# Optimization experiments

Hardware: AMD Instinct MI355X
Metric: run time of the kernel (lower is better)

## Reference

```python
import jax, jax.numpy as jnp
import numpy as np

N = 50000      # nodes
E = 800000     # edges (avg degree 16)
DIN = 128      # input_dim
DG = 128       # gnn_dim
DCLS = 128     # cls_dim
DOUT = 10      # output_dim
LMDA = 1.0     # rw_lmda
P_DROP = 0.5


def setup_inputs() -> dict:
    key = jax.random.key(0)
    ks = jax.random.split(key, 12)
    x = jax.random.normal(ks[0], (N, DIN), jnp.float32)
    edge_index = jax.random.randint(ks[1], (2, E), 0, N, dtype=jnp.int64)
    edge_weight = jax.random.uniform(ks[2], (E,), jnp.float32)
    def glorot(k, shape):
        lim = np.sqrt(6.0 / (shape[0] + shape[1])).astype(np.float32)
        return jax.random.uniform(k, shape, jnp.float32, -lim, lim)
    return dict(
        x=x, edge_index=edge_index, edge_weight=edge_weight,
        W_lin_in=glorot(ks[3], (DIN, DG)), b_lin_in=jnp.zeros((DG,), jnp.float32),
        W_agg_in=glorot(ks[4], (DG + DIN, DG)), b_agg_in=jnp.zeros((DG,), jnp.float32),
        W_lin_h=glorot(ks[5], (DG, DG)), b_lin_h=jnp.zeros((DG,), jnp.float32),
        W_agg_h=glorot(ks[6], (2 * DG, DG)), b_agg_h=jnp.zeros((DG,), jnp.float32),
        W_mlp1=glorot(ks[7], (DG, DCLS)), b_mlp1=jnp.zeros((DCLS,), jnp.float32),
        W_mlp2=glorot(ks[8], (DCLS, DOUT)), b_mlp2=jnp.zeros((DOUT,), jnp.float32),
    )


def _gs_layer(x, row, col, ew, inv_cnt, W_lin, b_lin, W_agg, b_agg):
    # GS_reweight: message = (1-lmda)*lin(x_j) + lmda*ew*lin(x_j), mean-aggregated
    # at row (flow='target_to_source': gather from col, scatter to row).
    h = x @ W_lin + b_lin                      # [N, DG] (lin before gather == lin(x_j))
    hj = h[col]                                # [E, DG] gather
    m = (1.0 - LMDA) * hj + LMDA * (ew[:, None] * hj)
    agg = jax.ops.segment_sum(m, row, num_segments=N) * inv_cnt[:, None]  # mean
    out = jnp.concatenate([agg, x], axis=-1) @ W_agg + b_agg              # update()
    return jax.nn.relu(out)


def _dropout(x, k):
    mask = jax.random.bernoulli(k, 1.0 - P_DROP, x.shape)
    return jnp.where(mask, x / (1.0 - P_DROP), 0.0)


def reference(x, edge_index, edge_weight,
              W_lin_in, b_lin_in, W_agg_in, b_agg_in,
              W_lin_h, b_lin_h, W_agg_h, b_agg_h,
              W_mlp1, b_mlp1, W_mlp2, b_mlp2):
    row, col = edge_index[0], edge_index[1]
    cnt = jax.ops.segment_sum(jnp.ones((E,), x.dtype), row, num_segments=N)
    inv_cnt = 1.0 / jnp.maximum(cnt, 1.0)     # scatter_mean: empty rows -> 0
    dk = jax.random.split(jax.random.key(42), 3)
    h = _gs_layer(x, row, col, edge_weight, inv_cnt, W_lin_in, b_lin_in, W_agg_in, b_agg_in)
    h = _dropout(jax.nn.relu(h), dk[0])       # relu is idempotent after update's relu
    for i in range(2):                        # layers 2,3 share prop_hidden weights
        h = _gs_layer(h, row, col, edge_weight, inv_cnt, W_lin_h, b_lin_h, W_agg_h, b_agg_h)
        h = _dropout(jax.nn.relu(h), dk[i + 1])
    y = jax.nn.relu(h @ W_mlp1 + b_mlp1) @ W_mlp2 + b_mlp2  # cls_layers=2, bn=False
    return (h, y)
```

## Files before the change

### kernel.cpp

```cpp
#include <hip/hip_runtime.h>
#include <cstdint>
#include <cstddef>


#define N_NODES 50000
#define N_EDGES 800000
#define DGN 128
#define DOUT 10
#define NELEM (N_NODES * DGN)
#define NMASKW (NELEM / 64)
#define NBINS 391
#define TILE 4096
#define NTILES ((N_EDGES + TILE - 1) / TILE)
#define GBF ((N_NODES + 63) / 64)
#define MK_BLOCKS 25000

#define XB_BLK 6250
#define HI_BLK NTILES
#define WC_BLK 128
#define TR_BLK 192
#define R0 XB_BLK
#define R1 (R0 + HI_BLK)
#define R2 (R1 + WC_BLK)
#define R3 (R2 + TR_BLK)
#define MEGA_BLOCKS (R3 + 1)

#define AB_BLOCKS ((N_NODES + 3) / 4)

typedef __attribute__((ext_vector_type(8))) short bf16x8;
typedef __attribute__((ext_vector_type(4))) float f32x4;

__host__ __device__ static inline unsigned short f2bf(float f) {
  union { float f; unsigned u; } c; c.f = f;
  unsigned u = c.u;
  return (unsigned short)((u + 0x7fffu + ((u >> 16) & 1u)) >> 16);
}
__device__ static inline float bflo(unsigned u) { return __uint_as_float(u << 16); }
__device__ static inline float bfhi(unsigned u) { return __uint_as_float(u & 0xffff0000u); }
__device__ static inline float bf2f(unsigned short h) {
  return __uint_as_float(((unsigned)h) << 16);
}

__host__ __device__ static inline void tf2x32(unsigned k0, unsigned k1,
                                              unsigned c0, unsigned c1,
                                              unsigned& o0, unsigned& o1) {
  unsigned ks2 = k0 ^ k1 ^ 0x1BD11BDAu;
  unsigned x0 = c0 + k0;
  unsigned x1 = c1 + k1;
#define TFR(r) { x0 += x1; x1 = (x1 << (r)) | (x1 >> (32 - (r))); x1 ^= x0; }
  TFR(13) TFR(15) TFR(26) TFR(6)
  x0 += k1;  x1 += ks2 + 1u;
  TFR(17) TFR(29) TFR(16) TFR(24)
  x0 += ks2; x1 += k0 + 2u;
  TFR(13) TFR(15) TFR(26) TFR(6)
  x0 += k0;  x1 += k1 + 3u;
  TFR(17) TFR(29) TFR(16) TFR(24)
  x0 += k1;  x1 += ks2 + 4u;
  TFR(13) TFR(15) TFR(26) TFR(6)
  x0 += ks2; x1 += k0 + 5u;
#undef TFR
  o0 = x0; o1 = x1;
}

__device__ static inline void mask_chunk(unsigned long long* __restrict__ gm,
                                         int i, unsigned k0, unsigned k1) {
  unsigned o0, o1;
  tf2x32(k0, k1, 0u, (unsigned)i, o0, o1);
  unsigned long long b = __ballot(((o0 ^ o1) >> 31) == 0u);
  if ((threadIdx.x & 63) == 0) gm[i >> 6] = b;
}

__global__ __launch_bounds__(256) void mega_kernel(
    const float* __restrict__ x, unsigned short* __restrict__ xb,
    const int* __restrict__ ei, int* __restrict__ chist,
    const float* __restrict__ Wli, const float* __restrict__ Wai,
    const float* __restrict__ Wlh, const float* __restrict__ Wah,
    const float* __restrict__ Wm1,
    const float* __restrict__ bli, const float* __restrict__ blh,
    unsigned short* __restrict__ Tai, unsigned short* __restrict__ Tah,
    unsigned short* __restrict__ Tm1,
    float* __restrict__ bvi, float* __restrict__ bvh) {
  __shared__ int h[NBINS];
  const int b = blockIdx.x;
  const int tid = threadIdx.x;

  if (b < R0) {
    int g = b * 256 + tid;
    float4 v = ((const float4*)x)[g];
    ushort4 o;
    o.x = f2bf(v.x); o.y = f2bf(v.y); o.z = f2bf(v.z); o.w = f2bf(v.w);
    ((ushort4*)xb)[g] = o;
  } else if (b < R1) {
    for (int i = tid; i < NBINS; i += 256) h[i] = 0;
    __syncthreads();
    const int e0 = (b - R0) * TILE;
#pragma unroll 4
    for (int j = 0; j < TILE; j += 256) {
      int e = e0 + j + tid;
      if (e < N_EDGES) {
        int r = ei[e];
        r = (r < 0) ? 0 : (r >= N_NODES ? N_NODES - 1 : r);
        atomicAdd(&h[r >> 7], 1);
      }
    }
    __syncthreads();
    for (int i = tid; i < NBINS; i += 256)
      if (h[i]) atomicAdd(&chist[i], h[i]);
  } else if (b < R2) {
    int idx = (b - R1) * 256 + tid;
    int n = idx & 127;
    int k = (idx >> 7) & 127;
    int m = idx >> 14;
    const float* Wl = m ? Wlh : Wli;
    const float* Wa = m ? Wah : Wai;
    unsigned short* T = m ? Tah : Tai;
    float acc = 0.0f;
#pragma unroll 8
    for (int j = 0; j < 128; ++j)
      acc += Wl[k * 128 + j] * Wa[j * 128 + n];
    T[n * 256 + k] = f2bf(acc);
  } else if (b < R3) {
    int j = (b - R2) * 256 + tid;
    if (j < 16384) {
      int kk = j & 127, n = j >> 7;
      Tai[n * 256 + 128 + kk] = f2bf(Wai[(size_t)(128 + kk) * 128 + n]);
    } else if (j < 32768) {
      int q = j - 16384;
      int kk = q & 127, n = q >> 7;
      Tah[n * 256 + 128 + kk] = f2bf(Wah[(size_t)(128 + kk) * 128 + n]);
    } else {
      int q = j - 32768;
      int k = q & 127, n = q >> 7;
      Tm1[n * 128 + k] = f2bf(Wm1[(size_t)k * 128 + n]);
    }
  } else {
    int n = tid & 127;
    const float* bl = (tid < 128) ? bli : blh;
    const float* Wa = (tid < 128) ? Wai : Wah;
    float acc = 0.0f;
    for (int j = 0; j < 128; ++j) acc += bl[j] * Wa[j * 128 + n];
    if (tid < 128) bvi[n] = acc; else bvh[n] = acc;
  }
}

__global__ __launch_bounds__(512) void prefix_kernel(const int* __restrict__ chist,
                                                     int* __restrict__ cbase,
                                                     int* __restrict__ ccursor,
                                                     int* __restrict__ rowptr) {
  __shared__ int s[512];
  const int t = threadIdx.x;
  int v = (t < NBINS) ? chist[t] : 0;
  s[t] = v;
  __syncthreads();
  for (int off = 1; off < 512; off <<= 1) {
    int tv = (t >= off) ? s[t - off] : 0;
    __syncthreads();
    s[t] += tv;
    __syncthreads();
  }
  if (t <= NBINS) {
    int ex = (t == 0) ? 0 : s[t - 1];
    cbase[t] = ex;
    if (t < NBINS) ccursor[t] = ex;
  }
  if (t == 0) rowptr[N_NODES] = N_EDGES;
}

__global__ __launch_bounds__(256) void scatter_kernel(const int* __restrict__ ei,
                                                      const float* __restrict__ ew,
                                                      int* __restrict__ ccursor,
                                                      uint2* __restrict__ pk,
                                                      unsigned long long* __restrict__ mg0,
                                                      unsigned k00, unsigned k01) {
  if (blockIdx.x >= NTILES) {
    mask_chunk(mg0, (blockIdx.x - NTILES) * 256 + threadIdx.x, k00, k01);
    return;
  }
  __shared__ uint2 st[TILE];
  __shared__ unsigned short sbin[TILE];
  __shared__ int h[NBINS];
  __shared__ int base[NBINS];
  __shared__ int gbase[NBINS];
  __shared__ int cur[NBINS];
  __shared__ int sc[512];
  const int tid = threadIdx.x;
  const int e0 = blockIdx.x * TILE;
  const int nt = (N_EDGES - e0 < TILE) ? (N_EDGES - e0) : TILE;

  for (int i = tid; i < NBINS; i += 256) { h[i] = 0; cur[i] = 0; }
  __syncthreads();
  for (int j = tid; j < nt; j += 256) {
    int r = ei[e0 + j];
    r = (r < 0) ? 0 : (r >= N_NODES ? N_NODES - 1 : r);
    atomicAdd(&h[r >> 7], 1);
  }
  __syncthreads();
  sc[tid] = (tid < NBINS) ? h[tid] : 0;
  sc[tid + 256] = (tid + 256 < NBINS) ? h[tid + 256] : 0;
  __syncthreads();
  for (int off = 1; off < 512; off <<= 1) {
    int a0 = (tid >= off) ? sc[tid - off] : 0;
    int a1 = (tid + 256 >= off) ? sc[tid + 256 - off] : 0;
    __syncthreads();
    sc[tid] += a0; sc[tid + 256] += a1;
    __syncthreads();
  }
  if (tid < NBINS) {
    base[tid] = sc[tid] - h[tid];
    if (h[tid]) gbase[tid] = atomicAdd(&ccursor[tid], h[tid]);
  }
  if (tid + 256 < NBINS) {
    base[tid + 256] = sc[tid + 256] - h[tid + 256];
    if (h[tid + 256]) gbase[tid + 256] = atomicAdd(&ccursor[tid + 256], h[tid + 256]);
  }
  __syncthreads();
  for (int j = tid; j < nt; j += 256) {
    int r = ei[e0 + j];
    r = (r < 0) ? 0 : (r >= N_NODES ? N_NODES - 1 : r);
    int c = ei[N_EDGES + e0 + j];
    c = (c < 0) ? 0 : (c >= N_NODES ? N_NODES - 1 : c);
    int bb = r >> 7;
    int slot = base[bb] + atomicAdd(&cur[bb], 1);
    uint2 p;
    p.x = ((unsigned)r << 16) | (unsigned)c;
    p.y = __float_as_uint(ew[e0 + j]);
    st[slot] = p;
    sbin[slot] = (unsigned short)bb;
  }
  __syncthreads();
  for (int j = tid; j < nt; j += 256) {
    int bb = sbin[j];
    pk[gbase[bb] + (j - base[bb])] = st[j];
  }
}

__global__ __launch_bounds__(256) void place_kernel(const int* __restrict__ cbase,
                                                    const uint2* __restrict__ pk,
                                                    uint2* __restrict__ csr,
                                                    int* __restrict__ rowptr,
                                                    float* __restrict__ invc) {
  __shared__ int lcnt[128];
  __shared__ int lpre[128];
  __shared__ int lcur[128];
  __shared__ int sc[128];
  const int b = blockIdx.x;
  const int tid = threadIdx.x;
  const int cb = cbase[b];
  const int n = cbase[b + 1] - cb;
  const int r0 = b << 7;
  const int nr = (N_NODES - r0 < 128) ? (N_NODES - r0) : 128;

  if (tid < 128) { lcnt[tid] = 0; lcur[tid] = 0; }
  __syncthreads();
  for (int i = tid; i < n; i += 256) {
    int r7 = (int)(pk[cb + i].x >> 16) - r0;
    atomicAdd(&lcnt[r7], 1);
  }
  __syncthreads();
  if (tid < 128) sc[tid] = lcnt[tid];
  __syncthreads();
  for (int off = 1; off < 128; off <<= 1) {
    int tv = (tid >= off && tid < 128) ? sc[tid - off] : 0;
    __syncthreads();
    if (tid < 128) sc[tid] += tv;
    __syncthreads();
  }
  if (tid < 128) lpre[tid] = sc[tid] - lcnt[tid];
  __syncthreads();
  if (tid < nr) {
    rowptr[r0 + tid] = cb + lpre[tid];
    int c = lcnt[tid];
    invc[r0 + tid] = 1.0f / (float)(c > 1 ? c : 1);
  }
  for (int i = tid; i < n; i += 256) {
    uint2 p = pk[cb + i];
    int r7 = (int)(p.x >> 16) - r0;
    int slot = cb + lpre[r7] + atomicAdd(&lcur[r7], 1);
    uint2 o;
    o.x = p.x & 0xFFFFu;
    o.y = p.y;
    csr[slot] = o;
  }
}

__global__ __launch_bounds__(256) void agg_kernel(const unsigned short* __restrict__ hlin,
                                                  const int* __restrict__ rowptr,
                                                  const uint2* __restrict__ csr,
                                                  const float* __restrict__ invc,
                                                  unsigned short* __restrict__ agg,
                                                  float* __restrict__ swout) {
  const int r = blockIdx.x * 4 + (threadIdx.x >> 6);
  const int lane = threadIdx.x & 63;
  const int es = lane >> 4;
  const int cg = lane & 15;
  const int start = rowptr[r];
  const int num = rowptr[r + 1] - start;
  const uint4* __restrict__ H = (const uint4*)hlin;

  float a[8] = {0.f, 0.f, 0.f, 0.f, 0.f, 0.f, 0.f, 0.f};
  float ws = 0.f;
  for (int e = 0; e < num; e += 16) {
#pragma unroll
    for (int j = 0; j < 4; ++j) {
      int idx = e + j * 4 + es;
      bool ok = idx < num;
      int idxc = ok ? idx : (num - 1);
      uint2 q = csr[start + idxc];
      float w = ok ? __uint_as_float(q.y) : 0.0f;
      uint4 p = H[(size_t)q.x * 16 + cg];
      ws += w;
      a[0] += w * bflo(p.x); a[1] += w * bfhi(p.x);
      a[2] += w * bflo(p.y); a[3] += w * bfhi(p.y);
      a[4] += w * bflo(p.z); a[5] += w * bfhi(p.z);
      a[6] += w * bflo(p.w); a[7] += w * bfhi(p.w);
    }
  }
#pragma unroll
  for (int k = 0; k < 8; ++k) {
    a[k] += __shfl_xor(a[k], 32);
    a[k] += __shfl_xor(a[k], 16);
  }
  ws += __shfl_xor(ws, 32);
  ws += __shfl_xor(ws, 16);
  const float s = invc[r];
  if (es == 0) {
    uint4 o;
    o.x = (unsigned)f2bf(a[0] * s) | ((unsigned)f2bf(a[1] * s) << 16);
    o.y = (unsigned)f2bf(a[2] * s) | ((unsigned)f2bf(a[3] * s) << 16);
    o.z = (unsigned)f2bf(a[4] * s) | ((unsigned)f2bf(a[5] * s) << 16);
    o.w = (unsigned)f2bf(a[6] * s) | ((unsigned)f2bf(a[7] * s) << 16);
    ((uint4*)agg)[(size_t)r * 16 + cg] = o;
  }
  if (swout && lane == 0) swout[r] = ws * s;
}

template <bool WF32, bool MASKGEN>
__global__ __launch_bounds__(256) void layer_gemm(
    const unsigned short* __restrict__ Agg, const unsigned short* __restrict__ Hin,
    const unsigned short* __restrict__ Wt,
    const float* __restrict__ bvec, const float* __restrict__ bagg,
    const float* __restrict__ sw,
    const unsigned long long* __restrict__ maskw,
    float* __restrict__ outf, unsigned short* __restrict__ outb,
    unsigned long long* __restrict__ gm, unsigned gk0, unsigned gk1) {
  if (MASKGEN && blockIdx.x >= GBF) {
    mask_chunk(gm, (blockIdx.x - GBF) * 256 + threadIdx.x, gk0, gk1);
    return;
  }
  constexpr int LS = 72;
  __shared__ unsigned short Als[64 * LS];
  __shared__ unsigned short Bls[128 * LS];
  const int tid = threadIdx.x;
  const int m0 = blockIdx.x * 64;
  const int lane = tid & 63;
  const int wid = tid >> 6;
  const int wm = (wid >> 1) * 32;
  const int wn = (wid & 1) * 64;
  const int ln = lane & 15;
  const int lh = lane >> 4;
  const int sArow = tid >> 2;
  const int sAk = (tid & 3) * 16;
  const int sBcol = tid >> 1;
  const int sBk = (tid & 1) * 32;
  int arow = m0 + sArow;
  if (arow >= N_NODES) arow = N_NODES - 1;

  f32x4 acc[2][4];
#pragma unroll
  for (int i = 0; i < 2; ++i)
#pragma unroll
    for (int j = 0; j < 4; ++j)
#pragma unroll
      for (int r = 0; r < 4; ++r) acc[i][j][r] = 0.0f;

  for (int kb = 0; kb < 256; kb += 64) {
    const unsigned short* Asrc = (kb < 128) ? Agg : Hin;
    const unsigned short* ap = Asrc + (size_t)arow * 128 + (kb & 127) + sAk;
    unsigned short* al = &Als[sArow * LS + sAk];
    *(uint4*)(al + 0) = *(const uint4*)(ap + 0);
    *(uint4*)(al + 8) = *(const uint4*)(ap + 8);
    const unsigned short* bp = Wt + (size_t)sBcol * 256 + kb + sBk;
    unsigned short* bl = &Bls[sBcol * LS + sBk];
    *(uint4*)(bl + 0)  = *(const uint4*)(bp + 0);
    *(uint4*)(bl + 8)  = *(const uint4*)(bp + 8);
    *(uint4*)(bl + 16) = *(const uint4*)(bp + 16);
    *(uint4*)(bl + 24) = *(const uint4*)(bp + 24);
    __syncthreads();
#pragma unroll
    for (int ks = 0; ks < 64; ks += 32) {
      bf16x8 af[2], bfr[4];
#pragma unroll
      for (int i = 0; i < 2; ++i)
        af[i] = *(const bf16x8*)&Als[(wm + i * 16 + ln) * LS + ks + lh * 8];
#pragma unroll
      for (int j = 0; j < 4; ++j)
        bfr[j] = *(const bf16x8*)&Bls[(wn + j * 16 + ln) * LS + ks + lh * 8];
#pragma unroll
      for (int i = 0; i < 2; ++i)
#pragma unroll
        for (int j = 0; j < 4; ++j)
          acc[i][j] = __builtin_amdgcn_mfma_f32_16x16x32_bf16(af[i], bfr[j], acc[i][j], 0, 0, 0);
    }
    __syncthreads();
  }

  const int lm = lane >> 4;
  float bc[4], b2[4];
#pragma unroll
  for (int j = 0; j < 4; ++j) {
    int col = wn + j * 16 + ln;
    bc[j] = bvec[col];
    b2[j] = bagg[col];
  }
#pragma unroll
  for (int i = 0; i < 2; ++i) {
    const int lr0 = wm + i * 16 + lm * 4;
#pragma unroll
    for (int r = 0; r < 4; ++r) {
      const int row = m0 + lr0 + r;
      if (row >= N_NODES) continue;
      const float swr = sw[row];
      const unsigned long long mw = maskw[(size_t)row * 2 + (wn >> 6)];
#pragma unroll
      for (int j = 0; j < 4; ++j) {
        const int col = wn + j * 16 + ln;
        float v = acc[i][j][r] + swr * bc[j] + b2[j];
        v = fmaxf(v, 0.0f);
        v = ((mw >> (col & 63)) & 1ull) ? 2.0f * v : 0.0f;
        if (WF32) outf[(size_t)row * DGN + col] = v;
        outb[(size_t)row * DGN + col] = f2bf(v);
      }
    }
  }
}

__global__ __launch_bounds__(256) void mlp_gemm(
    const unsigned short* __restrict__ A0,
    const unsigned short* __restrict__ Wt,
    const float* __restrict__ b1,
    const float* __restrict__ W2, const float* __restrict__ b2,
    float* __restrict__ y) {
  constexpr int LS = 72;
  constexpr int LT = 132;
  __shared__ unsigned short Als[64 * LS];
  __shared__ unsigned short Bls[128 * LS];
  __shared__ unsigned short tT[64 * LT];
  __shared__ float Ws[128 * DOUT];
  __shared__ float bs[DOUT];
  const int tid = threadIdx.x;
  const int m0 = blockIdx.x * 64;
  const int lane = tid & 63;
  const int wid = tid >> 6;
  const int wm = (wid >> 1) * 32;
  const int wn = (wid & 1) * 64;
  const int ln = lane & 15;
  const int lh = lane >> 4;
  const int sArow = tid >> 2;
  const int sAk = (tid & 3) * 16;
  const int sBcol = tid >> 1;
  const int sBk = (tid & 1) * 32;
  int arow = m0 + sArow;
  if (arow >= N_NODES) arow = N_NODES - 1;

  for (int i = tid; i < 128 * DOUT; i += 256) Ws[i] = W2[i];
  if (tid < DOUT) bs[tid] = b2[tid];

  f32x4 acc[2][4];
#pragma unroll
  for (int i = 0; i < 2; ++i)
#pragma unroll
    for (int j = 0; j < 4; ++j)
#pragma unroll
      for (int r = 0; r < 4; ++r) acc[i][j][r] = 0.0f;

  for (int kb = 0; kb < 128; kb += 64) {
    const unsigned short* ap = A0 + (size_t)arow * 128 + kb + sAk;
    unsigned short* al = &Als[sArow * LS + sAk];
    *(uint4*)(al + 0) = *(const uint4*)(ap + 0);
    *(uint4*)(al + 8) = *(const uint4*)(ap + 8);
    const unsigned short* bp = Wt + (size_t)sBcol * 128 + kb + sBk;
    unsigned short* bl = &Bls[sBcol * LS + sBk];
    *(uint4*)(bl + 0)  = *(const uint4*)(bp + 0);
    *(uint4*)(bl + 8)  = *(const uint4*)(bp + 8);
    *(uint4*)(bl + 16) = *(const uint4*)(bp + 16);
    *(uint4*)(bl + 24) = *(const uint4*)(bp + 24);
    __syncthreads();
#pragma unroll
    for (int ks = 0; ks < 64; ks += 32) {
      bf16x8 af[2], bfr[4];
#pragma unroll
      for (int i = 0; i < 2; ++i)
        af[i] = *(const bf16x8*)&Als[(wm + i * 16 + ln) * LS + ks + lh * 8];
#pragma unroll
      for (int j = 0; j < 4; ++j)
        bfr[j] = *(const bf16x8*)&Bls[(wn + j * 16 + ln) * LS + ks + lh * 8];
#pragma unroll
      for (int i = 0; i < 2; ++i)
#pragma unroll
        for (int j = 0; j < 4; ++j)
          acc[i][j] = __builtin_amdgcn_mfma_f32_16x16x32_bf16(af[i], bfr[j], acc[i][j], 0, 0, 0);
    }
    __syncthreads();
  }

  const int lm = lane >> 4;
  float bcol[4];
#pragma unroll
  for (int j = 0; j < 4; ++j) bcol[j] = b1[wn + j * 16 + ln];
#pragma unroll
  for (int i = 0; i < 2; ++i) {
    const int lr0 = wm + i * 16 + lm * 4;
#pragma unroll
    for (int r = 0; r < 4; ++r) {
      const int lr = lr0 + r;
#pragma unroll
      for (int j = 0; j < 4; ++j) {
        const int col = wn + j * 16 + ln;
        float v = fmaxf(acc[i][j][r] + bcol[j], 0.0f);
        tT[lr * LT + col] = f2bf(v);
      }
    }
  }
  __syncthreads();

  if (tid < 64) {
    int row = m0 + tid;
    if (row < N_NODES) {
      float a2[DOUT];
#pragma unroll
      for (int c = 0; c < DOUT; ++c) a2[c] = bs[c];
      const unsigned short* tr = &tT[tid * LT];
#pragma unroll 8
      for (int k = 0; k < 128; ++k) {
        float tv = bf2f(tr[k]);
        const float* wr = &Ws[k * DOUT];
#pragma unroll
        for (int c = 0; c < DOUT; ++c) a2[c] += tv * wr[c];
      }
      float* yp = y + (size_t)row * DOUT;
#pragma unroll
      for (int c = 0; c < DOUT; ++c) yp[c] = a2[c];
    }
  }
}

extern "C" void kernel_launch(void* const* d_in, const int* in_sizes, int n_in,
                              void* d_out, int out_size, void* d_ws, size_t ws_size,
                              hipStream_t stream) {
  const float* x        = (const float*)d_in[0];
  const int*   ei       = (const int*)d_in[1];
  const float* ew       = (const float*)d_in[2];
  const float* W_lin_in = (const float*)d_in[3];
  const float* b_lin_in = (const float*)d_in[4];
  const float* W_agg_in = (const float*)d_in[5];
  const float* b_agg_in = (const float*)d_in[6];
  const float* W_lin_h  = (const float*)d_in[7];
  const float* b_lin_h  = (const float*)d_in[8];
  const float* W_agg_h  = (const float*)d_in[9];
  const float* b_agg_h  = (const float*)d_in[10];
  const float* W_mlp1   = (const float*)d_in[11];
  const float* b_mlp1   = (const float*)d_in[12];
  const float* W_mlp2   = (const float*)d_in[13];
  const float* b_mlp2   = (const float*)d_in[14];

  float* hout = (float*)d_out;
  float* yout = hout + (size_t)NELEM;

  char* p = (char*)d_ws;
  auto alloc = [&](size_t bytes) {
    char* q = p;
    p += (bytes + 255) & ~(size_t)255;
    return q;
  };
  int*   chist   = (int*)alloc((size_t)(NBINS + 1) * 4);
  int*   cbase   = (int*)alloc((size_t)(NBINS + 1) * 4);
  int*   ccursor = (int*)alloc((size_t)NBINS * 4);
  int*   rowptr  = (int*)alloc((size_t)(N_NODES + 1) * 4);
  float* invc    = (float*)alloc((size_t)N_NODES * 4);
  float* swv     = (float*)alloc((size_t)N_NODES * 4);
  uint2* pk      = (uint2*)alloc((size_t)N_EDGES * 8);
  uint2* csr     = (uint2*)alloc((size_t)N_EDGES * 8);
  unsigned short* xb   = (unsigned short*)alloc((size_t)NELEM * 2);
  unsigned short* aggb = (unsigned short*)alloc((size_t)NELEM * 2);
  unsigned short* hA   = (unsigned short*)alloc((size_t)NELEM * 2);
  unsigned short* hB   = (unsigned short*)alloc((size_t)NELEM * 2);
  unsigned long long* mw0 = (unsigned long long*)alloc((size_t)NMASKW * 8);
  unsigned long long* mw1 = (unsigned long long*)alloc((size_t)NMASKW * 8);
  unsigned long long* mw2 = (unsigned long long*)alloc((size_t)NMASKW * 8);
  unsigned short* Tai = (unsigned short*)alloc(32768 * 2);
  unsigned short* Tah = (unsigned short*)alloc(32768 * 2);
  unsigned short* Tm1 = (unsigned short*)alloc(16384 * 2);
  float* bvi = (float*)alloc(128 * 4);
  float* bvh = (float*)alloc(128 * 4);

  unsigned dk[3][2];
  for (unsigned i = 0; i < 3; ++i) tf2x32(0u, 42u, 0u, i, dk[i][0], dk[i][1]);

  hipMemsetAsync(chist, 0, (size_t)(NBINS + 1) * 4, stream);
  mega_kernel<<<MEGA_BLOCKS, 256, 0, stream>>>(
      x, xb, ei, chist, W_lin_in, W_agg_in, W_lin_h, W_agg_h, W_mlp1,
      b_lin_in, b_lin_h, Tai, Tah, Tm1, bvi, bvh);

  prefix_kernel<<<1, 512, 0, stream>>>(chist, cbase, ccursor, rowptr);
  scatter_kernel<<<NTILES + MK_BLOCKS, 256, 0, stream>>>(
      ei, ew, ccursor, pk, mw0, dk[0][0], dk[0][1]);
  place_kernel<<<NBINS, 256, 0, stream>>>(cbase, pk, csr, rowptr, invc);

  agg_kernel<<<AB_BLOCKS, 256, 0, stream>>>(xb, rowptr, csr, invc, aggb, swv);
  layer_gemm<false, true><<<GBF + MK_BLOCKS, 256, 0, stream>>>(
      aggb, xb, Tai, bvi, b_agg_in, swv, mw0, nullptr, hA,
      mw1, dk[1][0], dk[1][1]);

  agg_kernel<<<AB_BLOCKS, 256, 0, stream>>>(hA, rowptr, csr, invc, aggb, nullptr);
  layer_gemm<false, true><<<GBF + MK_BLOCKS, 256, 0, stream>>>(
      aggb, hA, Tah, bvh, b_agg_h, swv, mw1, nullptr, hB,
      mw2, dk[2][0], dk[2][1]);

  agg_kernel<<<AB_BLOCKS, 256, 0, stream>>>(hB, rowptr, csr, invc, aggb, nullptr);
  layer_gemm<true, false><<<GBF, 256, 0, stream>>>(
      aggb, hB, Tah, bvh, b_agg_h, swv, mw2, hout, hA,
      nullptr, 0, 0);

  mlp_gemm<<<GBF, 256, 0, stream>>>(hA, Tm1, b_mlp1, W_mlp2, b_mlp2, yout);
}
```

Before: 326.9 us.

## Partition node features into 32-column panels so aggregation gathers stay cache-resident

Stores bf16 node features as four column panels of 32 elements per node (panel-major) instead of row-major 128-wide rows. The aggregation kernel now runs one grid slice per panel, so each slice gathers from a 3.2 MB working set that fits better in L2/LLC. Consumers (layer GEMM A-operand load, outputs, MLP GEMM) are rewritten to read and write the panel layout. The cost is four passes over the CSR edge list and narrower 64-byte gathers per edge.

```diff
diff --git a/kernel.cpp b/kernel.cpp
--- a/kernel.cpp
+++ b/kernel.cpp
@@ -14,6 +14,7 @@
 #define NTILES ((N_EDGES + TILE - 1) / TILE)
 #define GBF ((N_NODES + 63) / 64)
 #define MK_BLOCKS 25000
+#define PSTRIDE (N_NODES * 32)
 
 #define XB_BLK 6250
 #define HI_BLK NTILES
@@ -25,7 +26,9 @@
 #define R3 (R2 + TR_BLK)
 #define MEGA_BLOCKS (R3 + 1)
 
-#define AB_BLOCKS ((N_NODES + 3) / 4)
+#define AGG_RPB 16
+#define AGG_PB (N_NODES / AGG_RPB)
+#define AGG_BLOCKS (4 * AGG_PB)
 
 typedef __attribute__((ext_vector_type(8))) short bf16x8;
 typedef __attribute__((ext_vector_type(4))) float f32x4;
@@ -89,7 +92,9 @@
     float4 v = ((const float4*)x)[g];
     ushort4 o;
     o.x = f2bf(v.x); o.y = f2bf(v.y); o.z = f2bf(v.z); o.w = f2bf(v.w);
-    ((ushort4*)xb)[g] = o;
+    int node = g >> 5;
+    int d0 = (g & 31) << 2;
+    ((ushort4*)xb)[((size_t)(d0 >> 5) * PSTRIDE + (size_t)node * 32 + (d0 & 31)) >> 2] = o;
   } else if (b < R1) {
     for (int i = tid; i < NBINS; i += 256) h[i] = 0;
     __syncthreads();
@@ -283,55 +288,74 @@
   }
 }
 
-__global__ __launch_bounds__(256) void agg_kernel(const unsigned short* __restrict__ hlin,
-                                                  const int* __restrict__ rowptr,
-                                                  const uint2* __restrict__ csr,
-                                                  const float* __restrict__ invc,
-                                                  unsigned short* __restrict__ agg,
-                                                  float* __restrict__ swout) {
-  const int r = blockIdx.x * 4 + (threadIdx.x >> 6);
+__global__ __launch_bounds__(256) void agg_kernel(
+    const unsigned short* __restrict__ hlin,
+    const int* __restrict__ rowptr,
+    const uint2* __restrict__ csr,
+    const float* __restrict__ invc,
+    unsigned short* __restrict__ agg,
+    float* __restrict__ swout) {
+  const int p = blockIdx.x / AGG_PB;
+  const int rb = (blockIdx.x - p * AGG_PB) * AGG_RPB;
   const int lane = threadIdx.x & 63;
-  const int es = lane >> 4;
-  const int cg = lane & 15;
-  const int start = rowptr[r];
-  const int num = rowptr[r + 1] - start;
-  const uint4* __restrict__ H = (const uint4*)hlin;
-
-  float a[8] = {0.f, 0.f, 0.f, 0.f, 0.f, 0.f, 0.f, 0.f};
-  float ws = 0.f;
-  for (int e = 0; e < num; e += 16) {
-#pragma unroll
-    for (int j = 0; j < 4; ++j) {
-      int idx = e + j * 4 + es;
-      bool ok = idx < num;
-      int idxc = ok ? idx : (num - 1);
-      uint2 q = csr[start + idxc];
-      float w = ok ? __uint_as_float(q.y) : 0.0f;
-      uint4 p = H[(size_t)q.x * 16 + cg];
-      ws += w;
-      a[0] += w * bflo(p.x); a[1] += w * bfhi(p.x);
-      a[2] += w * bflo(p.y); a[3] += w * bfhi(p.y);
-      a[4] += w * bflo(p.z); a[5] += w * bfhi(p.z);
-      a[6] += w * bflo(p.w); a[7] += w * bfhi(p.w);
-    }
-  }
-#pragma unroll
-  for (int k = 0; k < 8; ++k) {
-    a[k] += __shfl_xor(a[k], 32);
-    a[k] += __shfl_xor(a[k], 16);
-  }
-  ws += __shfl_xor(ws, 32);
-  ws += __shfl_xor(ws, 16);
-  const float s = invc[r];
-  if (es == 0) {
-    uint4 o;
-    o.x = (unsigned)f2bf(a[0] * s) | ((unsigned)f2bf(a[1] * s) << 16);
-    o.y = (unsigned)f2bf(a[2] * s) | ((unsigned)f2bf(a[3] * s) << 16);
-    o.z = (unsigned)f2bf(a[4] * s) | ((unsigned)f2bf(a[5] * s) << 16);
-    o.w = (unsigned)f2bf(a[6] * s) | ((unsigned)f2bf(a[7] * s) << 16);
-    ((uint4*)agg)[(size_t)r * 16 + cg] = o;
-  }
-  if (swout && lane == 0) swout[r] = ws * s;
+  const int wid = threadIdx.x >> 6;
+  const int half = lane >> 5;
+  const int ec = (lane >> 2) & 7;
+  const int cg = lane & 3;
+  const uint4* __restrict__ H = (const uint4*)hlin + (size_t)p * (N_NODES * 4);
+
+  for (int rr = 0; rr < 2; ++rr) {
+    const int r = rb + wid * 4 + rr * 2 + half;
+    const int start = rowptr[r];
+    const int num = rowptr[r + 1] - start;
+    float a[8] = {0.f, 0.f, 0.f, 0.f, 0.f, 0.f, 0.f, 0.f};
+    float ws = 0.f;
+    for (int e = 0; e < num; e += 16) {
+      const int i1 = e + ec;
+      const int i2 = e + 8 + ec;
+      if (i1 < num) {
+        uint2 q = csr[start + i1];
+        float w = __uint_as_float(q.y);
+        uint4 pv = H[(size_t)q.x * 4 + cg];
+        ws += w;
+        a[0] += w * bflo(pv.x); a[1] += w * bfhi(pv.x);
+        a[2] += w * bflo(pv.y); a[3] += w * bfhi(pv.y);
+        a[4] += w * bflo(pv.z); a[5] += w * bfhi(pv.z);
+        a[6] += w * bflo(pv.w); a[7] += w * bfhi(pv.w);
+      }
+      if (i2 < num) {
+        uint2 q = csr[start + i2];
+        float w = __uint_as_float(q.y);
+        uint4 pv = H[(size_t)q.x * 4 + cg];
+        ws += w;
+        a[0] += w * bflo(pv.x); a[1] += w * bfhi(pv.x);
+        a[2] += w * bflo(pv.y); a[3] += w * bfhi(pv.y);
+        a[4] += w * bflo(pv.z); a[5] += w * bfhi(pv.z);
+        a[6] += w * bflo(pv.w); a[7] += w * bfhi(pv.w);
+      }
+    }
+#pragma unroll
+    for (int k = 0; k < 8; ++k) {
+      a[k] += __shfl_xor(a[k], 4);
+      a[k] += __shfl_xor(a[k], 8);
+      a[k] += __shfl_xor(a[k], 16);
+    }
+    const float s = invc[r];
+    if ((lane & 31) < 4) {
+      uint4 o;
+      o.x = (unsigned)f2bf(a[0] * s) | ((unsigned)f2bf(a[1] * s) << 16);
+      o.y = (unsigned)f2bf(a[2] * s) | ((unsigned)f2bf(a[3] * s) << 16);
+      o.z = (unsigned)f2bf(a[4] * s) | ((unsigned)f2bf(a[5] * s) << 16);
+      o.w = (unsigned)f2bf(a[6] * s) | ((unsigned)f2bf(a[7] * s) << 16);
+      ((uint4*)agg)[(size_t)r * 16 + p * 4 + cg] = o;
+    }
+    if (swout != nullptr && p == 0) {
+      ws += __shfl_xor(ws, 4);
+      ws += __shfl_xor(ws, 8);
+      ws += __shfl_xor(ws, 16);
+      if ((lane & 31) == 0) swout[r] = ws * s;
+    }
+  }
 }
 
 template <bool WF32, bool MASKGEN>
@@ -374,8 +398,13 @@
       for (int r = 0; r < 4; ++r) acc[i][j][r] = 0.0f;
 
   for (int kb = 0; kb < 256; kb += 64) {
-    const unsigned short* Asrc = (kb < 128) ? Agg : Hin;
-    const unsigned short* ap = Asrc + (size_t)arow * 128 + (kb & 127) + sAk;
+    const unsigned short* ap;
+    if (kb < 128) {
+      ap = Agg + (size_t)arow * 128 + kb + sAk;
+    } else {
+      int kk = kb - 128 + sAk;
+      ap = Hin + (size_t)(kk >> 5) * PSTRIDE + (size_t)arow * 32 + (kk & 31);
+    }
     unsigned short* al = &Als[sArow * LS + sAk];
     *(uint4*)(al + 0) = *(const uint4*)(ap + 0);
     *(uint4*)(al + 8) = *(const uint4*)(ap + 8);
@@ -428,7 +457,7 @@
         v = fmaxf(v, 0.0f);
         v = ((mw >> (col & 63)) & 1ull) ? 2.0f * v : 0.0f;
         if (WF32) outf[(size_t)row * DGN + col] = v;
-        outb[(size_t)row * DGN + col] = f2bf(v);
+        outb[(size_t)(col >> 5) * PSTRIDE + (size_t)row * 32 + (col & 31)] = f2bf(v);
       }
     }
   }
@@ -474,7 +503,9 @@
       for (int r = 0; r < 4; ++r) acc[i][j][r] = 0.0f;
 
   for (int kb = 0; kb < 128; kb += 64) {
-    const unsigned short* ap = A0 + (size_t)arow * 128 + kb + sAk;
+    int kk = kb + sAk;
+    const unsigned short* ap =
+        A0 + (size_t)(kk >> 5) * PSTRIDE + (size_t)arow * 32 + (kk & 31);
     unsigned short* al = &Als[sArow * LS + sAk];
     *(uint4*)(al + 0) = *(const uint4*)(ap + 0);
     *(uint4*)(al + 8) = *(const uint4*)(ap + 8);
@@ -606,17 +637,17 @@
       ei, ew, ccursor, pk, mw0, dk[0][0], dk[0][1]);
   place_kernel<<<NBINS, 256, 0, stream>>>(cbase, pk, csr, rowptr, invc);
 
-  agg_kernel<<<AB_BLOCKS, 256, 0, stream>>>(xb, rowptr, csr, invc, aggb, swv);
+  agg_kernel<<<AGG_BLOCKS, 256, 0, stream>>>(xb, rowptr, csr, invc, aggb, swv);
   layer_gemm<false, true><<<GBF + MK_BLOCKS, 256, 0, stream>>>(
       aggb, xb, Tai, bvi, b_agg_in, swv, mw0, nullptr, hA,
       mw1, dk[1][0], dk[1][1]);
 
-  agg_kernel<<<AB_BLOCKS, 256, 0, stream>>>(hA, rowptr, csr, invc, aggb, nullptr);
+  agg_kernel<<<AGG_BLOCKS, 256, 0, stream>>>(hA, rowptr, csr, invc, aggb, nullptr);
   layer_gemm<false, true><<<GBF + MK_BLOCKS, 256, 0, stream>>>(
       aggb, hA, Tah, bvh, b_agg_h, swv, mw1, nullptr, hB,
       mw2, dk[2][0], dk[2][1]);
 
-  agg_kernel<<<AB_BLOCKS, 256, 0, stream>>>(hB, rowptr, csr, invc, aggb, nullptr);
+  agg_kernel<<<AGG_BLOCKS, 256, 0, stream>>>(hB, rowptr, csr, invc, aggb, nullptr);
   layer_gemm<true, false><<<GBF, 256, 0, stream>>>(
       aggb, hB, Tah, bvh, b_agg_h, swv, mw2, hout, hA,
       nullptr, 0, 0);
```

Result: slower. 365.3 us (+11.7%).
